# Kernel optimization log

Measured on AMD Instinct MI355X. Metric: run time of the kernel, lower is better.

Reference implementation:

```python
import jax, jax.numpy as jnp
import numpy as np

B, S, D, H = 2, 4096, 512, 8
DK = D // H


def setup_inputs() -> dict:
    key = jax.random.key(0)
    ks = jax.random.split(key, 8)
    q = jax.random.normal(ks[0], (B, S, D), dtype=jnp.float32)
    k = jax.random.normal(ks[1], (B, S, D), dtype=jnp.float32)
    v = jax.random.normal(ks[2], (B, S, D), dtype=jnp.float32)
    mask = jax.random.randint(ks[3], (B, S, S), 0, 2, dtype=jnp.int32)
    scale = 1.0 / np.sqrt(D)
    w_q = jax.random.normal(ks[4], (D, D), dtype=jnp.float32) * scale
    w_k = jax.random.normal(ks[5], (D, D), dtype=jnp.float32) * scale
    w_v = jax.random.normal(ks[6], (D, D), dtype=jnp.float32) * scale
    w_o = jax.random.normal(ks[7], (D, D), dtype=jnp.float32) * scale
    return {"q": q, "k": k, "v": v, "mask": mask,
            "w_q": w_q, "w_k": w_k, "w_v": w_v, "w_o": w_o}


def reference(q, k, v, mask, w_q, w_k, w_v, w_o):
    # Projections (weights stored as [in, out]; no bias, matching bias=False)
    # [B,S,D] -> [B,H,S,DK]
    def split_heads(x):
        return x.reshape(B, S, H, DK).transpose(0, 2, 1, 3)

    qh = split_heads(q @ w_q)
    kh = split_heads(k @ w_k)
    vh = split_heads(v @ w_v)

    inv_sqrt_dk = jnp.float32(1.0 / np.sqrt(DK))
    # Explicit O(S^2) score matrix, as in the original module
    scores = jnp.einsum('bhqd,bhkd->bhqk', qh, kh) * inv_sqrt_dk
    scores = jnp.where(mask[:, None, :, :] == 0, jnp.float32(-1e9), scores)
    attn = jax.nn.softmax(scores, axis=-1)
    # dropout in eval mode (p=0) -> identity
    x = jnp.einsum('bhqk,bhkd->bhqd', attn, vh)
    x = x.transpose(0, 2, 1, 3).reshape(B, S, D)
    return x @ w_o
```

## Files before the change

### kernel.cpp

```cpp
#include <hip/hip_runtime.h>
#include <hip/hip_bf16.h>

#define Bn 2
#define Sn 4096
#define Dn 512
#define Hn 8
#define DKn 64

typedef __attribute__((ext_vector_type(8))) short bf16x8;
typedef __attribute__((ext_vector_type(4))) float f32x4;
typedef __attribute__((ext_vector_type(4))) _Float16 f16x4;
typedef __attribute__((ext_vector_type(8))) _Float16 f16x8;
typedef __attribute__((ext_vector_type(2))) _Float16 f16x2;
typedef __attribute__((ext_vector_type(8))) unsigned short us8;
typedef __attribute__((ext_vector_type(4))) unsigned short us4;

__device__ __forceinline__ unsigned short f2bf(float f) {
  unsigned u = __builtin_bit_cast(unsigned, f);
  u += 0x7fffu + ((u >> 16) & 1u);
  return (unsigned short)(u >> 16);
}

__device__ __forceinline__ unsigned cvtpk_bf16(float lo, float hi) {
  unsigned r;
  asm("v_cvt_pk_bf16_f32 %0, %1, %2" : "=v"(r) : "v"(lo), "v"(hi));
  return r;
}

__device__ __forceinline__ unsigned spread4(unsigned x) {
  x = (x | (x << 12)) & 0x000F000Fu;
  x = (x | (x << 6)) & 0x03030303u;
  x = (x | (x << 3)) & 0x11111111u;
  return x;
}

__global__ __launch_bounds__(256) void prep_k(
    const int* __restrict__ mask, unsigned int* __restrict__ pm,
    const float* __restrict__ wq, const float* __restrict__ wk,
    const float* __restrict__ wv, const float* __restrict__ wo,
    unsigned short* __restrict__ wt) {
  const int t = threadIdx.x;
  if (blockIdx.x < 256) {
    __shared__ unsigned short ls[64][68];
    int bid = blockIdx.x;
    int z = bid >> 6, x = bid & 7, y = (bid >> 3) & 7;
    const float* W = z == 0 ? wq : z == 1 ? wk : z == 2 ? wv : wo;
    const float wsc = (z == 0) ? 0.18033688011112042f : 1.0f;
    int k0 = x * 64, n0 = y * 64;
    for (int j = 0; j < 4; ++j) {
      int i = t + j * 256;
      int r = i >> 4, c4 = (i & 15) << 2;
      float4 f = *(const float4*)&W[(size_t)(k0 + r) * 512 + n0 + c4];
      ls[c4 + 0][r] = f2bf(f.x * wsc);
      ls[c4 + 1][r] = f2bf(f.y * wsc);
      ls[c4 + 2][r] = f2bf(f.z * wsc);
      ls[c4 + 3][r] = f2bf(f.w * wsc);
    }
    __syncthreads();
    unsigned short* out = wt + (size_t)z * 512 * 512;
    for (int j = 0; j < 4; ++j) {
      int i = t + j * 256;
      int r = i >> 4, c4 = (i & 15) << 2;
      us4 v = {ls[r][c4], ls[r][c4 + 1], ls[r][c4 + 2], ls[r][c4 + 3]};
      *(us4*)&out[(size_t)(n0 + r) * 512 + k0 + c4] = v;
    }
  } else {
    size_t gt = (size_t)(blockIdx.x - 256) * 256 + t;
    for (int it = 0; it < 8; ++it, gt += 1048576) {
      size_t e0 = gt * 4;
      int4 mv = *(const int4*)&mask[e0];
      unsigned long long bl0 = __ballot(mv.x != 0);
      unsigned long long bl1 = __ballot(mv.y != 0);
      unsigned long long bl2 = __ballot(mv.z != 0);
      unsigned long long bl3 = __ballot(mv.w != 0);
      if ((t & 63) < 8) {
        int wd = t & 7;
        unsigned word = spread4((unsigned)(bl0 >> (wd * 8)) & 0xFFu) |
                        (spread4((unsigned)(bl1 >> (wd * 8)) & 0xFFu) << 1) |
                        (spread4((unsigned)(bl2 >> (wd * 8)) & 0xFFu) << 2) |
                        (spread4((unsigned)(bl3 >> (wd * 8)) & 0xFFu) << 3);
        size_t eb = e0 & ~(size_t)255;
        int qq = (int)((eb >> 12) & 4095);
        int bb = (int)(eb >> 24);
        int kvw = (int)((eb >> 5) & 127) + wd;
        pm[((size_t)bb * 128 + kvw) * 4096 + qq] = word;
      }
    }
  }
}

template <int MT, bool HEADS>
__global__ __launch_bounds__(256, 2) void gemm_k(
    const float* __restrict__ aq, const float* __restrict__ ak,
    const float* __restrict__ av, const unsigned short* __restrict__ abf,
    const unsigned short* __restrict__ wt, unsigned short* __restrict__ oh,
    unsigned short* __restrict__ vtg, float* __restrict__ olin) {
  __shared__ unsigned short smem[MT * 8192 + 16384];
  const int z = blockIdx.z;
  const float* A32 = HEADS ? (z == 0 ? aq : z == 1 ? ak : av) : nullptr;
  const unsigned short* Wt = wt + (size_t)z * 512 * 512;
  const int m0 = blockIdx.x * (MT * 64), n0 = blockIdx.y * 128;
  const int t = threadIdx.x, w = t >> 6, l = t & 63;
  const int quad = l >> 4, c = l & 15;

  f32x4 acc[MT][8] = {};
  us8 apre[MT * 2], bpre[4];

  auto ldA = [&](int j, int kk) -> us8 {
    int i = t + j * 256, r = i >> 3, u = i & 7;
    if constexpr (HEADS) {
      const float* s = &A32[(size_t)(m0 + r) * 512 + kk + (u << 3)];
      float4 f0 = *(const float4*)s;
      float4 f1 = *(const float4*)(s + 4);
      uint4 p;
      p.x = cvtpk_bf16(f0.x, f0.y);
      p.y = cvtpk_bf16(f0.z, f0.w);
      p.z = cvtpk_bf16(f1.x, f1.y);
      p.w = cvtpk_bf16(f1.z, f1.w);
      return __builtin_bit_cast(us8, p);
    } else {
      return *(const us8*)&abf[(size_t)(m0 + r) * 512 + kk + (u << 3)];
    }
  };

#pragma unroll
  for (int j = 0; j < MT * 2; ++j) apre[j] = ldA(j, 0);
#pragma unroll
  for (int j = 0; j < 4; ++j) {
    int i = t + j * 256, r = i >> 3, u = i & 7;
    bpre[j] = *(const us8*)&Wt[(size_t)(n0 + r) * 512 + (u << 3)];
  }
#pragma unroll
  for (int j = 0; j < MT * 2; ++j) {
    int i = t + j * 256, r = i >> 3, u = i & 7;
    *(us8*)&smem[r * 64 + ((u ^ (r & 7)) << 3)] = apre[j];
  }
#pragma unroll
  for (int j = 0; j < 4; ++j) {
    int i = t + j * 256, r = i >> 3, u = i & 7;
    *(us8*)&smem[MT * 8192 + r * 64 + ((u ^ (r & 7)) << 3)] = bpre[j];
  }

  for (int k0 = 0; k0 < 512; k0 += 64) {
    const int cur = (k0 >> 6) & 1;
    const unsigned short* AsC = &smem[cur * (MT * 4096)];
    const unsigned short* BsC = &smem[MT * 8192 + cur * 8192];
    __syncthreads();
    const bool nxt = k0 + 64 < 512;
    if (nxt) {
#pragma unroll
      for (int j = 0; j < MT * 2; ++j) apre[j] = ldA(j, k0 + 64);
#pragma unroll
      for (int j = 0; j < 4; ++j) {
        int i = t + j * 256, r = i >> 3, u = i & 7;
        bpre[j] = *(const us8*)&Wt[(size_t)(n0 + r) * 512 + k0 + 64 + (u << 3)];
      }
    }

#pragma unroll
    for (int kc = 0; kc < 2; ++kc) {
      bf16x8 aA[MT], bB[8];
      int u = kc * 4 + quad;
#pragma unroll
      for (int mt = 0; mt < MT; ++mt) {
        int row = w * (MT * 16) + mt * 16 + c;
        aA[mt] = *(const bf16x8*)&AsC[row * 64 + ((u ^ (c & 7)) << 3)];
      }
#pragma unroll
      for (int nt = 0; nt < 8; ++nt) {
        int row = nt * 16 + c;
        bB[nt] = *(const bf16x8*)&BsC[row * 64 + ((u ^ (c & 7)) << 3)];
      }
      __builtin_amdgcn_s_setprio(1);
#pragma unroll
      for (int mt = 0; mt < MT; ++mt)
#pragma unroll
        for (int nt = 0; nt < 8; ++nt)
          acc[mt][nt] = __builtin_amdgcn_mfma_f32_16x16x32_bf16(
              aA[mt], bB[nt], acc[mt][nt], 0, 0, 0);
      __builtin_amdgcn_s_setprio(0);
    }

    if (nxt) {
      unsigned short* AsN = &smem[(cur ^ 1) * (MT * 4096)];
      unsigned short* BsN = &smem[MT * 8192 + (cur ^ 1) * 8192];
#pragma unroll
      for (int j = 0; j < MT * 2; ++j) {
        int i = t + j * 256, r = i >> 3, u = i & 7;
        *(us8*)&AsN[r * 64 + ((u ^ (r & 7)) << 3)] = apre[j];
      }
#pragma unroll
      for (int j = 0; j < 4; ++j) {
        int i = t + j * 256, r = i >> 3, u = i & 7;
        *(us8*)&BsN[r * 64 + ((u ^ (r & 7)) << 3)] = bpre[j];
      }
    }
  }

  if constexpr (HEADS) {
    if (z == 2) {
      __syncthreads();
#pragma unroll
      for (int mt = 0; mt < MT; ++mt) {
        int mb = w * (MT * 16) + mt * 16 + (quad << 2);
        int ml = (mb & 64) | (((mb >> 5) & 1) << 5) | (((mb >> 2) & 3) << 3) |
                 (((mb >> 4) & 1) << 2);
#pragma unroll
        for (int nt = 0; nt < 8; ++nt) {
          int nl = nt * 16 + c;
          us4 pk;
#pragma unroll
          for (int r = 0; r < 4; ++r)
            pk[r] = __builtin_bit_cast(unsigned short, (_Float16)acc[mt][nt][r]);
          *(us4*)&smem[nl * 152 + ml] = pk;
        }
      }
      __syncthreads();
      const int bb = m0 >> 12, sb = m0 & 4095;
#pragma unroll
      for (int j = 0; j < MT * 4; ++j) {
        int i = t + j * 256;
        int nl = i >> 4, mc = (i & 15) << 3;
        us8 vv = *(const us8*)&smem[nl * 152 + mc];
        int n = n0 + nl, hh = n >> 6, dk = n & 63;
        *(us8*)&vtg[((size_t)(bb * Hn + hh) * DKn + dk) * Sn + sb + mc] = vv;
      }
    } else {
#pragma unroll
      for (int mt = 0; mt < MT; ++mt)
#pragma unroll
        for (int nt = 0; nt < 8; ++nt) {
          int m = m0 + w * (MT * 16) + mt * 16 + (quad << 2);
          int n = n0 + nt * 16 + c;
          int b = m >> 12, s = m & 4095, hh = n >> 6, dk = n & 63;
          unsigned short* dst = &oh[(size_t)z * (Bn * Hn * Sn * DKn) +
                                    ((size_t)(b * Hn + hh) * Sn + s) * DKn + dk];
          unsigned pk0 = cvtpk_bf16(acc[mt][nt][0], acc[mt][nt][1]);
          unsigned pk1 = cvtpk_bf16(acc[mt][nt][2], acc[mt][nt][3]);
          dst[0] = (unsigned short)pk0;
          dst[DKn] = (unsigned short)(pk0 >> 16);
          dst[2 * DKn] = (unsigned short)pk1;
          dst[3 * DKn] = (unsigned short)(pk1 >> 16);
        }
    }
  } else {
#pragma unroll
    for (int mt = 0; mt < MT; ++mt)
#pragma unroll
      for (int nt = 0; nt < 8; ++nt)
#pragma unroll
        for (int r = 0; r < 4; ++r) {
          int m = m0 + w * (MT * 16) + mt * 16 + (quad << 2) + r;
          int n = n0 + nt * 16 + c;
          olin[(size_t)m * 512 + n] = acc[mt][nt][r];
        }
  }
}

__global__ __launch_bounds__(512, 4) void flash_k(
    const unsigned short* __restrict__ Qh, const unsigned short* __restrict__ Kh,
    const unsigned short* __restrict__ VtG, const unsigned int* __restrict__ pmt,
    unsigned short* __restrict__ attn) {
  __shared__ unsigned short Ks[2][2][32 * 64];
  __shared__ unsigned short Vts[2][2][64 * 32];
  __shared__ unsigned int Mw[2][2][128];
  __shared__ unsigned long long MskT[16];

  const int bid = blockIdx.x;
  const int h = bid & 7;
  const int b = (bid >> 3) & 1;
  const int q0 = (bid >> 4) * 128;
  const int t = threadIdx.x;
  const int g = t >> 8, tg = t & 255;
  const int w = (t >> 6) & 3, l = t & 63;
  const int quad = l >> 4, c = l & 15;
  const size_t hb = (size_t)(b * Hn + h) * Sn * DKn;
  const unsigned short* Qg = Qh + hb;

  if (t < 16) {
    unsigned lo = ((t & 1) ? 0xFFFFu : 0u) | ((t & 2) ? 0xFFFF0000u : 0u);
    unsigned hi = ((t & 4) ? 0xFFFFu : 0u) | ((t & 8) ? 0xFFFF0000u : 0u);
    MskT[t] = ((unsigned long long)hi << 32) | lo;
  }

  bf16x8 bQ[2][2];
#pragma unroll
  for (int qf = 0; qf < 2; ++qf) {
    int qrow = q0 + w * 32 + qf * 16 + c;
#pragma unroll
    for (int kc = 0; kc < 2; ++kc)
      bQ[qf][kc] = *(const bf16x8*)&Qg[(size_t)qrow * 64 + kc * 32 + quad * 8];
  }

  f32x4 oacc[2][4] = {};
  f32x4 oaccl[2] = {};
  f16x8 vone8;
#pragma unroll
  for (int i = 0; i < 8; ++i) vone8[i] = (_Float16)1.0f;

  const int sr = tg >> 3, su = tg & 7;
  const int dkr = tg >> 2, pu = tg & 3;
  const int offK = sr * 64 + ((su ^ (sr & 7)) << 3);
  const int offV = dkr * 32 + ((pu ^ ((dkr >> 1) & 3)) << 3);

  const unsigned short* kp = Kh + hb + (size_t)(g * 32 + sr) * 64 + (su << 3);
  const unsigned short* vp = VtG + hb + (size_t)dkr * Sn + g * 32 + (pu << 3);
  const unsigned int* mp =
      pmt + ((size_t)b * 128 + g) * 4096 + q0 + (tg & 127);

  us8 kpre, vpre;
  unsigned mpre;
  kpre = *(const us8*)kp;
  vpre = *(const us8*)vp;
  mpre = (tg < 128) ? *mp : 0u;
  *(us8*)&Ks[g][0][offK] = kpre;
  *(us8*)&Vts[g][0][offV] = vpre;
  if (tg < 128) Mw[g][0][tg] = mpre;

  for (int it = 0; it < 64; ++it) {
    const int cur = it & 1;
    __syncthreads();
    const bool nxt = it + 1 < 64;
    if (nxt) {
      kp += 4096; vp += 64; mp += 8192;
      kpre = *(const us8*)kp;
      vpre = *(const us8*)vp;
      if (tg < 128) mpre = *mp;
    }

    f32x4 sacc[2][2] = {};
#pragma unroll
    for (int kc = 0; kc < 2; ++kc) {
      int u = kc * 4 + quad;
#pragma unroll
      for (int kvt = 0; kvt < 2; ++kvt) {
        int row = kvt * 16 + c;
        bf16x8 aK =
            *(const bf16x8*)&Ks[g][cur][row * 64 + ((u ^ (c & 7)) << 3)];
#pragma unroll
        for (int qf = 0; qf < 2; ++qf)
          sacc[qf][kvt] = __builtin_amdgcn_mfma_f32_16x16x32_bf16(
              aK, bQ[qf][kc], sacc[qf][kvt], 0, 0, 0);
      }
    }

    f16x8 ph[2];
#pragma unroll
    for (int qf = 0; qf < 2; ++qf) {
      int qloc = w * 32 + qf * 16 + c;
      unsigned wd = Mw[g][cur][qloc] >> (quad << 2);
      uint4 ww;
#pragma unroll
      for (int kvh = 0; kvh < 2; ++kvh) {
        const f32x4 s4 = sacc[qf][kvh];
        unsigned long long mk = MskT[(wd >> (kvh << 4)) & 15u];
        unsigned a = __builtin_bit_cast(
            unsigned, __builtin_amdgcn_cvt_pkrtz(
                          __builtin_amdgcn_exp2f(s4[0]),
                          __builtin_amdgcn_exp2f(s4[1])));
        unsigned bpk = __builtin_bit_cast(
            unsigned, __builtin_amdgcn_cvt_pkrtz(
                          __builtin_amdgcn_exp2f(s4[2]),
                          __builtin_amdgcn_exp2f(s4[3])));
        (&ww.x)[kvh * 2] = a & (unsigned)mk;
        (&ww.x)[kvh * 2 + 1] = bpk & (unsigned)(mk >> 32);
      }
      ph[qf] = __builtin_bit_cast(f16x8, ww);
    }

#pragma unroll
    for (int dkt = 0; dkt < 4; ++dkt) {
      int dk2 = dkt * 16 + c;
      f16x8 bV = __builtin_bit_cast(
          f16x8,
          *(const us8*)&Vts[g][cur][dk2 * 32 + ((quad ^ ((dk2 >> 1) & 3)) << 3)]);
#pragma unroll
      for (int qf = 0; qf < 2; ++qf)
        oacc[qf][dkt] = __builtin_amdgcn_mfma_f32_16x16x32_f16(
            ph[qf], bV, oacc[qf][dkt], 0, 0, 0);
    }
#pragma unroll
    for (int qf = 0; qf < 2; ++qf)
      oaccl[qf] = __builtin_amdgcn_mfma_f32_16x16x32_f16(
          ph[qf], vone8, oaccl[qf], 0, 0, 0);

    if (nxt) {
      const int nb = cur ^ 1;
      *(us8*)&Ks[g][nb][offK] = kpre;
      *(us8*)&Vts[g][nb][offV] = vpre;
      if (tg < 128) Mw[g][nb][tg] = mpre;
    }
  }

  __syncthreads();
  float* fs = (float*)&Ks[0][0][0];
  float* fl = (float*)&Vts[0][0][0];
#pragma unroll
  for (int qf = 0; qf < 2; ++qf) {
    if (g == 1) {
#pragma unroll
      for (int dkt = 0; dkt < 4; ++dkt)
        *(f32x4*)&fs[((dkt * 4 + w) * 64 + l) * 4] = oacc[qf][dkt];
      *(f32x4*)&fl[(w * 64 + l) * 4] = oaccl[qf];
    }
    __syncthreads();
    if (g == 0) {
      f32x4 l1 = *(const f32x4*)&fl[(w * 64 + l) * 4];
#pragma unroll
      for (int r = 0; r < 4; ++r) oaccl[qf][r] += l1[r];
#pragma unroll
      for (int dkt = 0; dkt < 4; ++dkt) {
        f32x4 o1 = *(const f32x4*)&fs[((dkt * 4 + w) * 64 + l) * 4];
#pragma unroll
        for (int r = 0; r < 4; ++r) oacc[qf][dkt][r] += o1[r];
      }
    }
    __syncthreads();
  }
  if (g == 0) {
#pragma unroll
    for (int qf = 0; qf < 2; ++qf)
#pragma unroll
      for (int r = 0; r < 4; ++r) {
        float invr = 1.0f / oaccl[qf][r];
        unsigned short* dst =
            &attn[((size_t)(b * Sn + q0 + w * 32 + qf * 16 + (quad << 2) + r)) * Dn +
                  h * 64 + c];
#pragma unroll
        for (int dkt = 0; dkt < 4; ++dkt)
          dst[dkt * 16] = f2bf(oacc[qf][dkt][r] * invr);
      }
  }
}

extern "C" void kernel_launch(void* const* d_in, const int* in_sizes, int n_in,
                              void* d_out, int out_size, void* d_ws,
                              size_t ws_size, hipStream_t stream) {
  const float* q = (const float*)d_in[0];
  const float* k = (const float*)d_in[1];
  const float* v = (const float*)d_in[2];
  const int* mask = (const int*)d_in[3];
  const float* wq = (const float*)d_in[4];
  const float* wk = (const float*)d_in[5];
  const float* wv = (const float*)d_in[6];
  const float* wo = (const float*)d_in[7];
  float* out = (float*)d_out;

  char* ws = (char*)d_ws;
  const size_t headN = (size_t)Bn * Hn * Sn * DKn;
  const size_t tensB = headN * 2;
  unsigned short* attn = (unsigned short*)ws;
  size_t off = 3 * tensB;
  unsigned short* qkv = (unsigned short*)(ws + off);
  off += 3 * tensB;
  unsigned short* wt = (unsigned short*)(ws + off);
  off += 4ull * 512 * 512 * 2;
  unsigned int* pm = (unsigned int*)(ws + off);

  prep_k<<<4352, 256, 0, stream>>>(mask, pm, wq, wk, wv, wo, wt);
  gemm_k<2, true><<<dim3(64, 4, 3), 256, 0, stream>>>(
      q, k, v, nullptr, wt, qkv, qkv + 2 * headN, nullptr);
  flash_k<<<dim3(512), 512, 0, stream>>>(qkv, qkv + headN,
                                         qkv + 2 * headN, pm, attn);
  gemm_k<1, false><<<dim3(128, 4, 1), 256, 0, stream>>>(
      nullptr, nullptr, nullptr, attn, wt + 3ull * 512 * 512, nullptr, nullptr,
      out);
}
```

Measured before the change: 348.9 us.

## Load GEMM weight fragments directly from global memory instead of LDS

The projection GEMM stops staging the weight (B) tile through shared memory and has each lane read its MFMA B fragments straight from global memory, relying on caches for reuse across the four waves. This cuts the LDS footprint, and the launch bound is raised to 4 blocks per CU to gain occupancy. In exchange, every wave re-reads the same weight data from global/L2 each k-step with no prefetch, which adds load latency into the MFMA loop. The register budget also gets tighter under the higher occupancy target.

Measured after the change: 451.7 us. 29.5% more time.

```diff
diff --git a/kernel.cpp b/kernel.cpp
--- a/kernel.cpp
+++ b/kernel.cpp
@@ -90,12 +90,12 @@
 }
 
 template <int MT, bool HEADS>
-__global__ __launch_bounds__(256, 2) void gemm_k(
+__global__ __launch_bounds__(256, 4) void gemm_k(
     const float* __restrict__ aq, const float* __restrict__ ak,
     const float* __restrict__ av, const unsigned short* __restrict__ abf,
     const unsigned short* __restrict__ wt, unsigned short* __restrict__ oh,
     unsigned short* __restrict__ vtg, float* __restrict__ olin) {
-  __shared__ unsigned short smem[MT * 8192 + 16384];
+  __shared__ unsigned short smem[HEADS ? 19456 : MT * 8192];
   const int z = blockIdx.z;
   const float* A32 = HEADS ? (z == 0 ? aq : z == 1 ? ak : av) : nullptr;
   const unsigned short* Wt = wt + (size_t)z * 512 * 512;
@@ -104,7 +104,7 @@
   const int quad = l >> 4, c = l & 15;
 
   f32x4 acc[MT][8] = {};
-  us8 apre[MT * 2], bpre[4];
+  us8 apre[MT * 2];
 
   auto ldA = [&](int j, int kk) -> us8 {
     int i = t + j * 256, r = i >> 3, u = i & 7;
@@ -123,38 +123,24 @@
     }
   };
 
+  const unsigned short* Bp = Wt + (size_t)(n0 + c) * 512 + (quad << 3);
+
 #pragma unroll
   for (int j = 0; j < MT * 2; ++j) apre[j] = ldA(j, 0);
-#pragma unroll
-  for (int j = 0; j < 4; ++j) {
-    int i = t + j * 256, r = i >> 3, u = i & 7;
-    bpre[j] = *(const us8*)&Wt[(size_t)(n0 + r) * 512 + (u << 3)];
-  }
 #pragma unroll
   for (int j = 0; j < MT * 2; ++j) {
     int i = t + j * 256, r = i >> 3, u = i & 7;
     *(us8*)&smem[r * 64 + ((u ^ (r & 7)) << 3)] = apre[j];
   }
-#pragma unroll
-  for (int j = 0; j < 4; ++j) {
-    int i = t + j * 256, r = i >> 3, u = i & 7;
-    *(us8*)&smem[MT * 8192 + r * 64 + ((u ^ (r & 7)) << 3)] = bpre[j];
-  }
 
   for (int k0 = 0; k0 < 512; k0 += 64) {
     const int cur = (k0 >> 6) & 1;
     const unsigned short* AsC = &smem[cur * (MT * 4096)];
-    const unsigned short* BsC = &smem[MT * 8192 + cur * 8192];
     __syncthreads();
     const bool nxt = k0 + 64 < 512;
     if (nxt) {
 #pragma unroll
       for (int j = 0; j < MT * 2; ++j) apre[j] = ldA(j, k0 + 64);
-#pragma unroll
-      for (int j = 0; j < 4; ++j) {
-        int i = t + j * 256, r = i >> 3, u = i & 7;
-        bpre[j] = *(const us8*)&Wt[(size_t)(n0 + r) * 512 + k0 + 64 + (u << 3)];
-      }
     }
 
 #pragma unroll
@@ -167,10 +153,8 @@
         aA[mt] = *(const bf16x8*)&AsC[row * 64 + ((u ^ (c & 7)) << 3)];
       }
 #pragma unroll
-      for (int nt = 0; nt < 8; ++nt) {
-        int row = nt * 16 + c;
-        bB[nt] = *(const bf16x8*)&BsC[row * 64 + ((u ^ (c & 7)) << 3)];
-      }
+      for (int nt = 0; nt < 8; ++nt)
+        bB[nt] = *(const bf16x8*)&Bp[(size_t)nt * 8192 + k0 + kc * 32];
       __builtin_amdgcn_s_setprio(1);
 #pragma unroll
       for (int mt = 0; mt < MT; ++mt)
@@ -183,16 +167,10 @@
 
     if (nxt) {
       unsigned short* AsN = &smem[(cur ^ 1) * (MT * 4096)];
-      unsigned short* BsN = &smem[MT * 8192 + (cur ^ 1) * 8192];
 #pragma unroll
       for (int j = 0; j < MT * 2; ++j) {
         int i = t + j * 256, r = i >> 3, u = i & 7;
         *(us8*)&AsN[r * 64 + ((u ^ (r & 7)) << 3)] = apre[j];
-      }
-#pragma unroll
-      for (int j = 0; j < 4; ++j) {
-        int i = t + j * 256, r = i >> 3, u = i & 7;
-        *(us8*)&BsN[r * 64 + ((u ^ (r & 7)) << 3)] = bpre[j];
       }
     }
   }
```
